# Performance work log

Hardware: AMD Instinct MI355X
Metric: run time of the kernel (lower is better)

The kernel has to match this reference:

```python
import jax, jax.numpy as jnp
import numpy as np

B, N, C = 8, 196, 512
NC, H = 10, 8
HD = C // H
SCALE = HD ** -0.5


def setup_inputs() -> dict:
    key = jax.random.key(0)
    ks = jax.random.split(key, 8)
    s = 1.0 / np.sqrt(C)
    return {
        "x": jax.random.normal(ks[0], (B, N, C), jnp.float32),
        "anchors": jax.random.normal(ks[1], (NC, N, C), jnp.float32),
        "weights": jax.random.uniform(ks[2], (B, H, NC), jnp.float32),
        "Wqk": jax.random.normal(ks[3], (C, C), jnp.float32) * s,
        "Wqk2": jax.random.normal(ks[4], (C, C), jnp.float32) * s,
        "Wv": jax.random.normal(ks[5], (C, C), jnp.float32) * s,
        "Wproj": jax.random.normal(ks[6], (C, C), jnp.float32) * s,
        "bproj": jax.random.normal(ks[7], (C,), jnp.float32) * 0.01,
    }


def _heads(t):
    # (..., N, C) -> (..., H, N, HD)
    shp = t.shape[:-2]
    return t.reshape(shp + (t.shape[-2], H, HD)).swapaxes(-3, -2)


def reference(x, anchors, weights, Wqk, Wqk2, Wv, Wproj, bproj):
    v = _heads(x @ Wv)                      # (B, H, N, HD)
    q = _heads(x @ Wqk)[:, None]            # (B, 1, H, N, HD)
    k = _heads(anchors @ Wqk)[None]         # (1, NC, H, N, HD)
    q2 = _heads(x @ Wqk2)[:, None]          # (B, 1, H, N, HD)
    k2 = _heads(anchors @ Wqk2)[None]       # (1, NC, H, N, HD)

    # ReLU-clipped double attention, both (B, NC, H, N, N)
    left_attn = jnp.maximum(-(q @ k.swapaxes(-2, -1)) * SCALE, 0.0)
    right_attn = jnp.maximum((k2 @ q2.swapaxes(-2, -1)) * SCALE, 0.0)

    attn = left_attn @ right_attn           # (B, NC, H, N, N)
    # per-head class-weighted combine: (B,H,NC) x (B,NC,H,N,N) -> (B,H,N,N)
    tmp = jnp.einsum('bhc,bchnm->bhnm', weights, attn)
    out = tmp @ v                           # (B, H, N, HD)
    # NOTE: original torch code reshapes (B,H,N,HD)->(B,N,C) WITHOUT a
    # transpose back; we replicate that exact flatten order.
    out = out.reshape(B, N, C)
    out = out @ Wproj + bproj
    return (out, left_attn)
```

## Files before the change

### kernel.cpp

```cpp
#include <hip/hip_runtime.h>

#define OFF_XB     0u
#define OFF_AB     1605632u
#define OFF_WQKT   3612672u
#define OFF_WQK2T  4136960u
#define OFF_WVT    4661248u
#define OFF_WPROJT 5185536u
#define OFF_XQ     5709824u
#define OFF_XQ2    7315456u
#define OFF_XV     8921088u
#define OFF_AQ     10526720u
#define OFF_AQ2    12533760u
#define OFF_RVT    14540800u
#define OFF_OUT1   35512320u
#define OFF_P      37117952u

typedef __attribute__((ext_vector_type(8))) short bf16x8;
typedef __attribute__((ext_vector_type(4))) float f32x4;
#define MFMA(a, b, c) __builtin_amdgcn_mfma_f32_16x16x32_bf16((a), (b), (c), 0, 0, 0)

__device__ __forceinline__ unsigned short f2bf(float x) {
  unsigned u = __builtin_bit_cast(unsigned, x);
  u += 0x7fffu + ((u >> 16) & 1u);
  return (unsigned short)(u >> 16);
}
__device__ __forceinline__ float bf2f(unsigned short s) {
  return __builtin_bit_cast(float, ((unsigned)s) << 16);
}

__device__ __forceinline__ void gl_lds16(const void* g, void* l) {
  __builtin_amdgcn_global_load_lds(
      (const __attribute__((address_space(1))) unsigned int*)g,
      (__attribute__((address_space(3))) unsigned int*)l, 16, 0, 0);
}

__device__ __forceinline__ void stage64(const unsigned short* g0, int stride,
                                        unsigned short (*T)[72], int tid, int nrows) {
  int wv = tid >> 6;
  char* base = (char*)&T[0][0];
#pragma unroll
  for (int i = 0; i < 2; i++) {
    int k = i * 256 + tid;
    int r = k / 9, c = k - r * 9;
    if (r < nrows)
      gl_lds16(g0 + (size_t)r * stride + (c << 3), base + (((i << 2) + wv) << 10));
  }
  if (tid < 64) {
    int k = 512 + tid;
    int r = k / 9, c = k - r * 9;
    if (r < nrows)
      gl_lds16(g0 + (size_t)r * stride + (c << 3), base + 8192);
  }
}

__device__ __forceinline__ void vload_T(uint4* va, uint4* vb, const unsigned short* __restrict__ g,
                                        int row0, int nrows, int col0, int tid) {
  int j0 = tid >> 3, d0 = (tid & 7) << 3;
  *va = make_uint4(0, 0, 0, 0);
  *vb = make_uint4(0, 0, 0, 0);
  if (j0 < nrows) *va = *(const uint4*)(g + (size_t)(row0 + j0) * 512 + col0 + d0);
  if (j0 + 32 < nrows) *vb = *(const uint4*)(g + (size_t)(row0 + j0 + 32) * 512 + col0 + d0);
}
__device__ __forceinline__ void vwrite_T(unsigned short T[64][72], uint4 va, uint4 vb, int tid) {
  int j0 = tid >> 3, d0 = (tid & 7) << 3;
  unsigned short s[8];
  *(uint4*)s = va;
#pragma unroll
  for (int u = 0; u < 8; u++) T[d0 + u][j0] = s[u];
  *(uint4*)s = vb;
#pragma unroll
  for (int u = 0; u < 8; u++) T[d0 + u][j0 + 32] = s[u];
}

__global__ __launch_bounds__(256) void pre_kernel(const float* __restrict__ x, const float* __restrict__ anchors,
                                                  const float* __restrict__ Wqk, const float* __restrict__ Wqk2,
                                                  const float* __restrict__ Wv, const float* __restrict__ Wproj,
                                                  char* __restrict__ ws) {
  int tid = threadIdx.x;
  if (blockIdx.x < 1764) {
    int base = blockIdx.x * 1024 + (tid << 2);
    float4 f = (base < 802816) ? *(const float4*)(x + base)
                               : *(const float4*)(anchors + (base - 802816));
    unsigned short s[4] = {f2bf(f.x), f2bf(f.y), f2bf(f.z), f2bf(f.w)};
    *(uint2*)((unsigned short*)(ws + OFF_XB) + base) = *(uint2*)s;
    return;
  }
  __shared__ __align__(16) unsigned short Ls[64][72];
  int idx = blockIdx.x - 1764;
  int wsel = idx >> 6, t = idx & 63;
  int k0 = (t >> 3) << 6, n0 = (t & 7) << 6;
  const float* W;
  unsigned short* WT;
  switch (wsel) {
    case 0:  W = Wqk;   WT = (unsigned short*)(ws + OFF_WQKT);   break;
    case 1:  W = Wqk2;  WT = (unsigned short*)(ws + OFF_WQK2T);  break;
    case 2:  W = Wv;    WT = (unsigned short*)(ws + OFF_WVT);    break;
    default: W = Wproj; WT = (unsigned short*)(ws + OFF_WPROJT); break;
  }
  {
    int r = tid >> 2, seg = (tid & 3) << 4;
    const float* p = W + (size_t)(k0 + r) * 512 + n0 + seg;
    float4 f0 = *(const float4*)p, f1 = *(const float4*)(p + 4);
    float4 f2 = *(const float4*)(p + 8), f3 = *(const float4*)(p + 12);
    unsigned short s[16] = {f2bf(f0.x), f2bf(f0.y), f2bf(f0.z), f2bf(f0.w),
                            f2bf(f1.x), f2bf(f1.y), f2bf(f1.z), f2bf(f1.w),
                            f2bf(f2.x), f2bf(f2.y), f2bf(f2.z), f2bf(f2.w),
                            f2bf(f3.x), f2bf(f3.y), f2bf(f3.z), f2bf(f3.w)};
    *(uint4*)&Ls[r][seg] = *(uint4*)s;
    *(uint4*)&Ls[r][seg + 8] = *(uint4*)(s + 8);
  }
  __syncthreads();
  {
    int r = tid >> 2, seg = (tid & 3) << 4;
    unsigned short s[16];
#pragma unroll
    for (int u = 0; u < 16; u++) s[u] = Ls[seg + u][r];
    unsigned short* dst = WT + (size_t)(n0 + r) * 512 + k0 + seg;
    *(uint4*)dst = *(uint4*)s;
    *(uint4*)(dst + 8) = *(uint4*)(s + 8);
  }
}

template <int NW>
__device__ __forceinline__ void proj_body(const unsigned short* __restrict__ A,
                                          const unsigned short* W0, const unsigned short* W1,
                                          const unsigned short* W2,
                                          unsigned short* O0, unsigned short* O1, unsigned short* O2,
                                          int M, unsigned short (*As)[72], unsigned short (*Wsh)[72]) {
  int row0 = (int)blockIdx.x << 6;
  if (row0 >= M) return;
  int col0 = (int)blockIdx.y << 6;
  int tid = threadIdx.x;
  int w = tid >> 6, lm = tid & 15, lq = (tid >> 4) & 3;
  const unsigned short* WTs[3] = {W0, W1, W2};
  unsigned short* Os[3] = {O0, O1, O2};
  f32x4 acc[NW][4] = {};
  for (int k0 = 0; k0 < 512; k0 += 64) {
    __syncthreads();
    stage64(A + (size_t)row0 * 512 + k0, 512, As, tid, 64);
#pragma unroll
    for (int ww = 0; ww < NW; ww++)
      stage64(WTs[ww] + (size_t)col0 * 512 + k0, 512,
              (unsigned short(*)[72])&Wsh[ww << 6], tid, 64);
    __syncthreads();
#pragma unroll
    for (int kk = 0; kk < 2; kk++) {
      bf16x8 af[4];
#pragma unroll
      for (int mi = 0; mi < 4; mi++)
        af[mi] = *(const bf16x8*)&As[(mi << 4) + lm][(kk << 5) + (lq << 3)];
#pragma unroll
      for (int ww = 0; ww < NW; ww++) {
        bf16x8 bf = *(const bf16x8*)&Wsh[(ww << 6) + (w << 4) + lm][(kk << 5) + (lq << 3)];
#pragma unroll
        for (int mi = 0; mi < 4; mi++) acc[ww][mi] = MFMA(af[mi], bf, acc[ww][mi]);
      }
    }
  }
  int ncol = col0 + (w << 4) + lm;
#pragma unroll
  for (int ww = 0; ww < NW; ww++)
#pragma unroll
    for (int mi = 0; mi < 4; mi++)
#pragma unroll
      for (int r2 = 0; r2 < 4; r2++) {
        int row = row0 + (mi << 4) + (lq << 2) + r2;
        if (row < M)
          Os[ww][(size_t)row * 512 + ncol] = f2bf(acc[ww][mi][r2]);
      }
}

__global__ __launch_bounds__(256) void proj_combo(char* __restrict__ ws) {
  __shared__ __align__(16) unsigned short As[64][72];
  __shared__ __align__(16) unsigned short Wsh[192][72];
  const unsigned short* xb = (const unsigned short*)(ws + OFF_XB);
  const unsigned short* ab = (const unsigned short*)(ws + OFF_AB);
  const unsigned short* wqkt  = (const unsigned short*)(ws + OFF_WQKT);
  const unsigned short* wqk2t = (const unsigned short*)(ws + OFF_WQK2T);
  const unsigned short* wvt   = (const unsigned short*)(ws + OFF_WVT);
  if (blockIdx.z == 0)
    proj_body<3>(xb, wqkt, wqk2t, wvt,
                 (unsigned short*)(ws + OFF_XQ), (unsigned short*)(ws + OFF_XQ2),
                 (unsigned short*)(ws + OFF_XV), 1568, As, Wsh);
  else
    proj_body<2>(ab, wqkt, wqk2t, nullptr,
                 (unsigned short*)(ws + OFF_AQ), (unsigned short*)(ws + OFF_AQ2),
                 nullptr, 1960, As, Wsh);
}

__global__ __launch_bounds__(256) void final_gemm(const unsigned short* __restrict__ out1,
                                                  const unsigned short* __restrict__ WT,
                                                  const float* __restrict__ bias, float* __restrict__ out) {
  __shared__ __align__(16) unsigned short As[64][72];
  __shared__ __align__(16) unsigned short Ws[64][72];
  int row0 = (int)blockIdx.x << 6;
  int col0 = (int)blockIdx.y << 6;
  int tid = threadIdx.x;
  int w = tid >> 6, lm = tid & 15, lq = (tid >> 4) & 3;
  f32x4 acc[4] = {};
  for (int k0 = 0; k0 < 512; k0 += 64) {
    __syncthreads();
    stage64(out1 + (size_t)row0 * 512 + k0, 512, As, tid, 64);
    stage64(WT + (size_t)col0 * 512 + k0, 512, Ws, tid, 64);
    __syncthreads();
#pragma unroll
    for (int kk = 0; kk < 2; kk++) {
      bf16x8 bf = *(const bf16x8*)&Ws[(w << 4) + lm][(kk << 5) + (lq << 3)];
#pragma unroll
      for (int mi = 0; mi < 4; mi++) {
        bf16x8 af = *(const bf16x8*)&As[(mi << 4) + lm][(kk << 5) + (lq << 3)];
        acc[mi] = MFMA(af, bf, acc[mi]);
      }
    }
  }
  int ncol = col0 + (w << 4) + lm;
  float bv = bias[ncol];
#pragma unroll
  for (int mi = 0; mi < 4; mi++)
#pragma unroll
    for (int r2 = 0; r2 < 4; r2++) {
      int row = row0 + (mi << 4) + (lq << 2) + r2;
      if (row < 1568)
        out[(size_t)row * 512 + ncol] = acc[mi][r2] + bv;
    }
}

__global__ __launch_bounds__(256) void rv_mfma(char* __restrict__ ws) {
  const unsigned short* xq2 = (const unsigned short*)(ws + OFF_XQ2);
  const unsigned short* aq2 = (const unsigned short*)(ws + OFF_AQ2);
  const unsigned short* xv  = (const unsigned short*)(ws + OFF_XV);
  unsigned short* rvt       = (unsigned short*)(ws + OFF_RVT);
  __shared__ __align__(16) unsigned short Qs[64][72];
  __shared__ __align__(16) unsigned short Vt[64][72];
  __shared__ __align__(16) unsigned short Ss[64][72];
  int d = blockIdx.x;
  int wk = ((d & 7) * 320) + (d >> 3);
  int it = wk & 3;
  int g = wk >> 2;
  int bh = g / 10, c = g - bh * 10;
  int b = bh >> 3, h = bh & 7;
  int bch = (b * 10 + c) * 8 + h;
  int i0 = it << 6;
  int tid = threadIdx.x;
  int w = tid >> 6, lm = tid & 15, lq = (tid >> 4) & 3;
  int iglob = i0 + (w << 4) + lm;

  bf16x8 kb[2] = {};
  if (iglob < 196) {
    const unsigned short* kp = aq2 + (size_t)(c * 196 + iglob) * 512 + (h << 6) + (lq << 3);
    kb[0] = *(const bf16x8*)kp;
    kb[1] = *(const bf16x8*)(kp + 32);
  }
  stage64(xq2 + (size_t)(b * 196) * 512 + (h << 6), 512, Qs, tid, 64);
  uint4 va, vb;
  vload_T(&va, &vb, xv, b * 196, 64, h << 6, tid);

  f32x4 acc[4] = {};
#pragma unroll
  for (int jt = 0; jt < 4; jt++) {
    int j0 = jt << 6;
    __syncthreads();
    vwrite_T(Vt, va, vb, tid);
    f32x4 s[4] = {};
#pragma unroll
    for (int kk = 0; kk < 2; kk++)
#pragma unroll
      for (int mj = 0; mj < 4; mj++) {
        bf16x8 af = *(const bf16x8*)&Qs[(mj << 4) + lm][(kk << 5) + (lq << 3)];
        s[mj] = MFMA(af, kb[kk], s[mj]);
      }
#pragma unroll
    for (int mj = 0; mj < 4; mj++) {
      unsigned short u[4] = {f2bf(fmaxf(0.125f * s[mj][0], 0.f)), f2bf(fmaxf(0.125f * s[mj][1], 0.f)),
                             f2bf(fmaxf(0.125f * s[mj][2], 0.f)), f2bf(fmaxf(0.125f * s[mj][3], 0.f))};
      *(uint2*)&Ss[(w << 4) + lm][(mj << 4) + (lq << 2)] = *(uint2*)u;
    }
    if (jt < 3) vload_T(&va, &vb, xv, b * 196 + j0 + 64, min(64, 196 - j0 - 64), h << 6, tid);
    __syncthreads();
    if (jt < 3) stage64(xq2 + (size_t)(b * 196 + j0 + 64) * 512 + (h << 6), 512, Qs, tid, 64);
#pragma unroll
    for (int kk = 0; kk < 2; kk++) {
      bf16x8 bf = *(const bf16x8*)&Vt[(w << 4) + lm][(kk << 5) + (lq << 3)];
#pragma unroll
      for (int mi = 0; mi < 4; mi++) {
        bf16x8 af = *(const bf16x8*)&Ss[(mi << 4) + lm][(kk << 5) + (lq << 3)];
        acc[mi] = MFMA(af, bf, acc[mi]);
      }
    }
  }
  __syncthreads();
#pragma unroll
  for (int mi = 0; mi < 4; mi++) {
    unsigned short u[4] = {f2bf(acc[mi][0]), f2bf(acc[mi][1]), f2bf(acc[mi][2]), f2bf(acc[mi][3])};
    *(uint2*)&Ss[(w << 4) + lm][(mi << 4) + (lq << 2)] = *(uint2*)u;
  }
  __syncthreads();
  {
    int dd = tid >> 2, seg = (tid & 3) << 4;
    unsigned short* dst = rvt + ((size_t)(bch * 4 + it) * 64 + dd) * 64 + seg;
    *(uint4*)dst = *(uint4*)&Ss[dd][seg];
    *(uint4*)(dst + 8) = *(uint4*)&Ss[dd][seg + 8];
  }
}

__global__ __launch_bounds__(256) void attn_mfma(char* __restrict__ ws, float* __restrict__ left,
                                                 unsigned short* __restrict__ P) {
  const unsigned short* xq  = (const unsigned short*)(ws + OFF_XQ);
  const unsigned short* aq  = (const unsigned short*)(ws + OFF_AQ);
  const unsigned short* rvt = (const unsigned short*)(ws + OFF_RVT);
  __shared__ __align__(16) unsigned short Ks[64][72];
  __shared__ __align__(16) unsigned short Ss[64][72];
  int d = blockIdx.x;
  int wk = ((d & 7) * 320) + (d >> 3);
  int i0 = (wk & 3) << 6;
  int g = wk >> 2;
  int c = g >> 6;
  int bh = g & 63;
  int b = bh >> 3, h = bh & 7;
  int bch = (b * 10 + c) * 8 + h;
  int tid = threadIdx.x;
  int w = tid >> 6, lm = tid & 15, lq = (tid >> 4) & 3;
  int iglob = i0 + (w << 4) + lm;

  bf16x8 qb[2];
  {
    const unsigned short* qp = xq + (size_t)(b * 196 + iglob) * 512 + (h << 6) + (lq << 3);
    qb[0] = *(const bf16x8*)qp;
    qb[1] = *(const bf16x8*)(qp + 32);
  }
  {
    uint4 z = make_uint4(0, 0, 0, 0);
    for (int k = tid; k < 540; k += 256)
      *(uint4*)((char*)&Ks[0][0] + 576 + k * 16) = z;
  }
  stage64(aq + (size_t)(c * 196 + 192) * 512 + (h << 6), 512, Ks, tid, 4);
  const unsigned short* rbase = rvt + (size_t)bch * 16384 + (((w << 4) + lm) << 6) + (lq << 3);
  bf16x8 rv0 = *(const bf16x8*)(rbase + 3 * 4096);
  bf16x8 rv1 = *(const bf16x8*)(rbase + 3 * 4096 + 32);

  f32x4 acc[4] = {};
  size_t lbase = (size_t)bch * (196 * 196);
#pragma unroll
  for (int t = 0; t < 4; t++) {
    int jt = (t == 0) ? 3 : t - 1;
    int j0 = jt << 6;
    __syncthreads();
    f32x4 s[4] = {};
#pragma unroll
    for (int kk = 0; kk < 2; kk++)
#pragma unroll
      for (int mj = 0; mj < 4; mj++) {
        bf16x8 af = *(const bf16x8*)&Ks[(mj << 4) + lm][(kk << 5) + (lq << 3)];
        s[mj] = MFMA(af, qb[kk], s[mj]);
      }
#pragma unroll
    for (int mj = 0; mj < 4; mj++) {
      f32x4 lv;
      lv[0] = fmaxf(-0.125f * s[mj][0], 0.f);
      lv[1] = fmaxf(-0.125f * s[mj][1], 0.f);
      lv[2] = fmaxf(-0.125f * s[mj][2], 0.f);
      lv[3] = fmaxf(-0.125f * s[mj][3], 0.f);
      int jloc = (mj << 4) + (lq << 2);
      if (iglob < 196 && j0 + jloc < 196)
        *(f32x4*)&left[lbase + (size_t)iglob * 196 + j0 + jloc] = lv;
      unsigned short u[4] = {f2bf(lv[0]), f2bf(lv[1]), f2bf(lv[2]), f2bf(lv[3])};
      *(uint2*)&Ss[(w << 4) + lm][jloc] = *(uint2*)u;
    }
    __syncthreads();
    if (t < 3)
      stage64(aq + (size_t)(c * 196 + (t << 6)) * 512 + (h << 6), 512, Ks, tid, 64);
    bf16x8 cur0 = rv0, cur1 = rv1;
    if (t < 3) {
      rv0 = *(const bf16x8*)(rbase + t * 4096);
      rv1 = *(const bf16x8*)(rbase + t * 4096 + 32);
    }
#pragma unroll
    for (int kk = 0; kk < 2; kk++) {
      bf16x8 bf = (kk == 0) ? cur0 : cur1;
#pragma unroll
      for (int mi = 0; mi < 4; mi++) {
        bf16x8 af = *(const bf16x8*)&Ss[(mi << 4) + lm][(kk << 5) + (lq << 3)];
        acc[mi] = MFMA(af, bf, acc[mi]);
      }
    }
  }
  __syncthreads();
#pragma unroll
  for (int mi = 0; mi < 4; mi++)
#pragma unroll
    for (int r = 0; r < 4; r++)
      Ss[(mi << 4) + (lq << 2) + r][(w << 4) + lm] = f2bf(acc[mi][r]);
  __syncthreads();
  {
    int row = tid >> 2, seg = (tid & 3) << 4;
    if (i0 + row < 196) {
      unsigned short* dst = P + ((size_t)(bh * 10 + c) * 196 + i0 + row) * 64 + seg;
      *(uint4*)dst = *(uint4*)&Ss[row][seg];
      *(uint4*)(dst + 8) = *(uint4*)&Ss[row][seg + 8];
    }
  }
}

__global__ __launch_bounds__(256) void reduce_out1(const unsigned short* __restrict__ P,
                                                   const float* __restrict__ weights,
                                                   unsigned short* __restrict__ out1) {
  int t = blockIdx.x * 256 + threadIdx.x;
  int base = t << 2;
  int bh = base / 12544;
  int rem = base - bh * 12544;
  const float* wrow = weights + bh * 10;
  float a0 = 0.f, a1 = 0.f, a2 = 0.f, a3 = 0.f;
#pragma unroll
  for (int c = 0; c < 10; c++) {
    float wc = wrow[c];
    const unsigned short* p = P + ((size_t)(bh * 10 + c)) * 12544 + rem;
    ushort4 u = *(const ushort4*)p;
    a0 = fmaf(wc, bf2f(u.x), a0);
    a1 = fmaf(wc, bf2f(u.y), a1);
    a2 = fmaf(wc, bf2f(u.z), a2);
    a3 = fmaf(wc, bf2f(u.w), a3);
  }
  unsigned short s[4] = {f2bf(a0), f2bf(a1), f2bf(a2), f2bf(a3)};
  *(uint2*)&out1[base] = *(uint2*)s;
}

extern "C" void kernel_launch(void* const* d_in, const int* in_sizes, int n_in,
                              void* d_out, int out_size, void* d_ws, size_t ws_size,
                              hipStream_t stream) {
  (void)in_sizes; (void)n_in; (void)out_size; (void)ws_size;
  const float* x       = (const float*)d_in[0];
  const float* anchors = (const float*)d_in[1];
  const float* weights = (const float*)d_in[2];
  const float* Wqk     = (const float*)d_in[3];
  const float* Wqk2    = (const float*)d_in[4];
  const float* Wv      = (const float*)d_in[5];
  const float* Wproj   = (const float*)d_in[6];
  const float* bproj   = (const float*)d_in[7];
  char* ws = (char*)d_ws;
  float* out  = (float*)d_out;
  float* left = out + 802816;

  dim3 blk(256);
  pre_kernel<<<dim3(2020), blk, 0, stream>>>(x, anchors, Wqk, Wqk2, Wv, Wproj, ws);
  proj_combo<<<dim3(31, 8, 2), blk, 0, stream>>>(ws);
  rv_mfma<<<dim3(2560), blk, 0, stream>>>(ws);
  attn_mfma<<<dim3(2560), blk, 0, stream>>>(ws, left, (unsigned short*)(ws + OFF_P));
  reduce_out1<<<dim3(784), blk, 0, stream>>>((const unsigned short*)(ws + OFF_P), weights,
                                             (unsigned short*)(ws + OFF_OUT1));
  final_gemm<<<dim3(25, 8), blk, 0, stream>>>((const unsigned short*)(ws + OFF_OUT1),
                                              (const unsigned short*)(ws + OFF_WPROJT), bproj, out);
}
```

Baseline: 218.9 us.

## Fuse fp32-to-bf16 activation conversion into projection GEMM and swizzle V transpose LDS

Removes the separate conversion pass that wrote bf16 copies of x and anchors to workspace. The projection GEMM now loads fp32 activations directly and converts them while staging into shared memory. This saves a round trip through global memory, but each projection block now reads twice the bytes per activation tile, and the conversion is repeated across the column blocks. Separately, the transposed V tile in LDS is written and read with an XOR swizzle to reduce bank conflicts from the strided scalar transpose writes.

```diff
diff --git a/kernel.cpp b/kernel.cpp
--- a/kernel.cpp
+++ b/kernel.cpp
@@ -53,6 +53,25 @@
   }
 }
 
+__device__ __forceinline__ void stageA_f32(unsigned short (*T)[72], const float* __restrict__ A,
+                                           int row0, int M, int k0, int tid) {
+  int r = tid >> 2, cs = (tid & 3) << 4;
+  float4 f0 = make_float4(0.f, 0.f, 0.f, 0.f), f1 = f0, f2 = f0, f3 = f0;
+  if (row0 + r < M) {
+    const float* p = A + (size_t)(row0 + r) * 512 + k0 + cs;
+    f0 = *(const float4*)p;
+    f1 = *(const float4*)(p + 4);
+    f2 = *(const float4*)(p + 8);
+    f3 = *(const float4*)(p + 12);
+  }
+  unsigned short s[16] = {f2bf(f0.x), f2bf(f0.y), f2bf(f0.z), f2bf(f0.w),
+                          f2bf(f1.x), f2bf(f1.y), f2bf(f1.z), f2bf(f1.w),
+                          f2bf(f2.x), f2bf(f2.y), f2bf(f2.z), f2bf(f2.w),
+                          f2bf(f3.x), f2bf(f3.y), f2bf(f3.z), f2bf(f3.w)};
+  *(uint4*)&T[r][cs] = *(uint4*)s;
+  *(uint4*)&T[r][cs + 8] = *(uint4*)(s + 8);
+}
+
 __device__ __forceinline__ void vload_T(uint4* va, uint4* vb, const unsigned short* __restrict__ g,
                                         int row0, int nrows, int col0, int tid) {
   int j0 = tid >> 3, d0 = (tid & 7) << 3;
@@ -63,30 +82,22 @@
 }
 __device__ __forceinline__ void vwrite_T(unsigned short T[64][72], uint4 va, uint4 vb, int tid) {
   int j0 = tid >> 3, d0 = (tid & 7) << 3;
+  int sw = (tid & 7) << 3;
   unsigned short s[8];
   *(uint4*)s = va;
 #pragma unroll
-  for (int u = 0; u < 8; u++) T[d0 + u][j0] = s[u];
+  for (int u = 0; u < 8; u++) T[d0 + u][j0 ^ sw] = s[u];
   *(uint4*)s = vb;
 #pragma unroll
-  for (int u = 0; u < 8; u++) T[d0 + u][j0 + 32] = s[u];
-}
-
-__global__ __launch_bounds__(256) void pre_kernel(const float* __restrict__ x, const float* __restrict__ anchors,
-                                                  const float* __restrict__ Wqk, const float* __restrict__ Wqk2,
+  for (int u = 0; u < 8; u++) T[d0 + u][(j0 + 32) ^ sw] = s[u];
+}
+
+__global__ __launch_bounds__(256) void pre_kernel(const float* __restrict__ Wqk, const float* __restrict__ Wqk2,
                                                   const float* __restrict__ Wv, const float* __restrict__ Wproj,
                                                   char* __restrict__ ws) {
+  __shared__ __align__(16) unsigned short Ls[64][72];
   int tid = threadIdx.x;
-  if (blockIdx.x < 1764) {
-    int base = blockIdx.x * 1024 + (tid << 2);
-    float4 f = (base < 802816) ? *(const float4*)(x + base)
-                               : *(const float4*)(anchors + (base - 802816));
-    unsigned short s[4] = {f2bf(f.x), f2bf(f.y), f2bf(f.z), f2bf(f.w)};
-    *(uint2*)((unsigned short*)(ws + OFF_XB) + base) = *(uint2*)s;
-    return;
-  }
-  __shared__ __align__(16) unsigned short Ls[64][72];
-  int idx = blockIdx.x - 1764;
+  int idx = blockIdx.x;
   int wsel = idx >> 6, t = idx & 63;
   int k0 = (t >> 3) << 6, n0 = (t & 7) << 6;
   const float* W;
@@ -122,7 +133,7 @@
 }
 
 template <int NW>
-__device__ __forceinline__ void proj_body(const unsigned short* __restrict__ A,
+__device__ __forceinline__ void proj_body(const float* __restrict__ A,
                                           const unsigned short* W0, const unsigned short* W1,
                                           const unsigned short* W2,
                                           unsigned short* O0, unsigned short* O1, unsigned short* O2,
@@ -137,7 +148,7 @@
   f32x4 acc[NW][4] = {};
   for (int k0 = 0; k0 < 512; k0 += 64) {
     __syncthreads();
-    stage64(A + (size_t)row0 * 512 + k0, 512, As, tid, 64);
+    stageA_f32(As, A, row0, M, k0, tid);
 #pragma unroll
     for (int ww = 0; ww < NW; ww++)
       stage64(WTs[ww] + (size_t)col0 * 512 + k0, 512,
@@ -170,20 +181,20 @@
       }
 }
 
-__global__ __launch_bounds__(256) void proj_combo(char* __restrict__ ws) {
+__global__ __launch_bounds__(256) void proj_combo(const float* __restrict__ x,
+                                                  const float* __restrict__ anchors,
+                                                  char* __restrict__ ws) {
   __shared__ __align__(16) unsigned short As[64][72];
   __shared__ __align__(16) unsigned short Wsh[192][72];
-  const unsigned short* xb = (const unsigned short*)(ws + OFF_XB);
-  const unsigned short* ab = (const unsigned short*)(ws + OFF_AB);
   const unsigned short* wqkt  = (const unsigned short*)(ws + OFF_WQKT);
   const unsigned short* wqk2t = (const unsigned short*)(ws + OFF_WQK2T);
   const unsigned short* wvt   = (const unsigned short*)(ws + OFF_WVT);
   if (blockIdx.z == 0)
-    proj_body<3>(xb, wqkt, wqk2t, wvt,
+    proj_body<3>(x, wqkt, wqk2t, wvt,
                  (unsigned short*)(ws + OFF_XQ), (unsigned short*)(ws + OFF_XQ2),
                  (unsigned short*)(ws + OFF_XV), 1568, As, Wsh);
   else
-    proj_body<2>(ab, wqkt, wqk2t, nullptr,
+    proj_body<2>(anchors, wqkt, wqk2t, nullptr,
                  (unsigned short*)(ws + OFF_AQ), (unsigned short*)(ws + OFF_AQ2),
                  nullptr, 1960, As, Wsh);
 }
@@ -278,9 +289,11 @@
     if (jt < 3) vload_T(&va, &vb, xv, b * 196 + j0 + 64, min(64, 196 - j0 - 64), h << 6, tid);
     __syncthreads();
     if (jt < 3) stage64(xq2 + (size_t)(b * 196 + j0 + 64) * 512 + (h << 6), 512, Qs, tid, 64);
+    int vrow = (w << 4) + lm;
+    int vsw = ((vrow >> 3) & 7) << 3;
 #pragma unroll
     for (int kk = 0; kk < 2; kk++) {
-      bf16x8 bf = *(const bf16x8*)&Vt[(w << 4) + lm][(kk << 5) + (lq << 3)];
+      bf16x8 bf = *(const bf16x8*)&Vt[vrow][((kk << 5) + (lq << 3)) ^ vsw];
 #pragma unroll
       for (int mi = 0; mi < 4; mi++) {
         bf16x8 af = *(const bf16x8*)&Ss[(mi << 4) + lm][(kk << 5) + (lq << 3)];
@@ -441,8 +454,8 @@
   float* left = out + 802816;
 
   dim3 blk(256);
-  pre_kernel<<<dim3(2020), blk, 0, stream>>>(x, anchors, Wqk, Wqk2, Wv, Wproj, ws);
-  proj_combo<<<dim3(31, 8, 2), blk, 0, stream>>>(ws);
+  pre_kernel<<<dim3(256), blk, 0, stream>>>(Wqk, Wqk2, Wv, Wproj, ws);
+  proj_combo<<<dim3(31, 8, 2), blk, 0, stream>>>(x, anchors, ws);
   rv_mfma<<<dim3(2560), blk, 0, stream>>>(ws);
   attn_mfma<<<dim3(2560), blk, 0, stream>>>(ws, left, (unsigned short*)(ws + OFF_P));
   reduce_out1<<<dim3(784), blk, 0, stream>>>((const unsigned short*)(ws + OFF_P), weights,
```

Result: faster. 206.3 us (-5.8%).
